# Optimization experiments

Hardware: AMD Instinct MI355X
Metric: run time of the kernel (lower is better)

## Reference

```python
import jax, jax.numpy as jnp
import numpy as np

# H36M 17-joint skeleton: parent-of array
_PARENTS = [-1, 0, 1, 2, 0, 4, 5, 0, 7, 8, 9, 8, 11, 12, 8, 14, 15]

def _make_triplets():
    # (jp, j, jc) for every joint j with a parent jp and child jc
    trips = []
    for jc, j in enumerate(_PARENTS):
        if j <= 0 and j != 0:
            continue
        if j == -1:
            continue
        jp = _PARENTS[j]
        if jp == -1:
            continue
        trips.append((jp, j, jc))
    return trips

TRIPLETS = _make_triplets()  # 12 fixed triplets

B, N, J, C = 16, 243, 17, 512
H, D = 8, C // 8
EPS = 1e-5


def setup_inputs() -> dict:
    key = jax.random.key(0)
    ks = jax.random.split(key, 5)
    s = 1.0 / np.sqrt(C)
    x = jax.random.normal(ks[0], (B, N, J, C), dtype=jnp.float32)
    Wqkv = jax.random.normal(ks[1], (C, 3 * C), dtype=jnp.float32) * s
    bqkv = jax.random.normal(ks[2], (3 * C,), dtype=jnp.float32) * 0.01
    Wproj = jax.random.normal(ks[3], (C, C), dtype=jnp.float32) * s
    bproj = jax.random.normal(ks[4], (C,), dtype=jnp.float32) * 0.01
    return {"x": x, "Wqkv": Wqkv, "bqkv": bqkv, "Wproj": Wproj, "bproj": bproj}


def _hsdm(x, Wqkv, bqkv, Wproj, bproj):
    # x: (B, N, J, C) -> tokens over joints per frame
    xf = x.reshape(B * N, J, C)
    qkv = xf @ Wqkv + bqkv                                   # (BN, J, 3C)
    qkv = qkv.reshape(B * N, J, 3, H, D).transpose(2, 0, 3, 1, 4)  # (3, BN, H, J, D)
    q, k, v = qkv[0], qkv[1], qkv[2]
    scale = 1.0 / jnp.sqrt(jnp.float32(D))
    attn = jax.nn.softmax(jnp.einsum('bhqd,bhkd->bhqk', q, k) * scale, axis=-1)
    # sequential hierarchical adjustment over fixed skeleton triplets
    # (order matters: later triplets read entries written by earlier ones)
    for jp, j, jc in TRIPLETS:
        half = attn[:, :, j, jp] * 0.5
        attn = attn.at[:, :, j, jc].add(half).at[:, :, jc, j].add(half)
    # dropout is identity at inference
    xa = jnp.einsum('bhqk,bhkd->bhqd', attn, v)              # (BN, H, J, D)
    xa = xa.transpose(0, 2, 1, 3).reshape(B * N, J, C)
    xa = xa @ Wproj + bproj
    y = x + xa.reshape(B, N, J, C)
    mu = jnp.mean(y, axis=-1, keepdims=True)
    var = jnp.var(y, axis=-1, keepdims=True)
    return (y - mu) / jnp.sqrt(var + EPS)                     # LN without affine


def reference(x, Wqkv, bqkv, Wproj, bproj):
    return _hsdm(x, Wqkv, bqkv, Wproj, bproj)
```

## Files before the change

kernel.cpp:

```cpp
#include <hip/hip_runtime.h>

typedef unsigned short u16;
typedef unsigned int u32;
typedef short bf16x8 __attribute__((ext_vector_type(8)));
typedef float f32x4 __attribute__((ext_vector_type(4)));
typedef float f32x16 __attribute__((ext_vector_type(16)));

#define M_ROWS   66096
#define M_PAD    66176
#define C_DIM    512
#define NQKV     1536
#define NFRAME   3888


__device__ __forceinline__ u16 f2bf(float f) {
    u32 u = __float_as_uint(f);
    u32 r = (u + 0x7fffu + ((u >> 16) & 1u)) >> 16;
    return (u16)r;
}
__device__ __forceinline__ float bf2f(u16 v) {
    return __uint_as_float(((u32)v) << 16);
}
__device__ __forceinline__ void async16(const void* g, void* l) {
    __builtin_amdgcn_global_load_lds(
        (const __attribute__((address_space(1))) unsigned int*)g,
        (__attribute__((address_space(3))) unsigned int*)l, 16, 0, 0);
}


__global__ __launch_bounds__(256) void cast_x(const float* __restrict__ x, u16* __restrict__ xb) {
    u32 cid = blockIdx.x * 256u + threadIdx.x;
    u32 m  = cid >> 6;
    u32 c0 = (cid & 63u) * 8u;
    if (m >= M_PAD) return;
    u16 v[8];
    if (m < M_ROWS) {
        const float* p = x + (size_t)m * C_DIM + c0;
        float4 f1 = *(const float4*)p;
        float4 f2 = *(const float4*)(p + 4);
        v[0]=f2bf(f1.x); v[1]=f2bf(f1.y); v[2]=f2bf(f1.z); v[3]=f2bf(f1.w);
        v[4]=f2bf(f2.x); v[5]=f2bf(f2.y); v[6]=f2bf(f2.z); v[7]=f2bf(f2.w);
    } else {
        #pragma unroll
        for (int i = 0; i < 8; ++i) v[i] = 0;
    }
    u16* dst = xb + ((size_t)(c0 >> 5) * M_PAD + m) * 32 + (c0 & 31u);
    *(uint4*)dst = *(const uint4*)v;
}


__global__ __launch_bounds__(256) void cast_w(const float* __restrict__ W, u16* __restrict__ out, int N) {
    __shared__ float tile[32 * 65];
    const int n0 = blockIdx.x * 64;
    const int kt = blockIdx.y;
    const int t  = threadIdx.x;
    for (int i = t; i < 2048; i += 256) {
        int k = i >> 6, n = i & 63;
        tile[k * 65 + n] = W[(size_t)(kt * 32 + k) * N + n0 + n];
    }
    __syncthreads();
    {
        int n = t >> 2, kk0 = (t & 3) * 8;
        u16 v[8];
        #pragma unroll
        for (int j = 0; j < 8; ++j) v[j] = f2bf(tile[(kk0 + j) * 65 + n]);
        u16* dst = out + ((size_t)kt * N + n0 + n) * 32 + kk0;
        *(uint4*)dst = *(const uint4*)v;
    }
}


__global__ __launch_bounds__(256) void gemm1(const u16* __restrict__ xb,
                                             const u16* __restrict__ wt,
                                             const float* __restrict__ bqkv,
                                             u16* __restrict__ qkv) {
    __shared__ u16 As[128 * 32];
    __shared__ u16 Bs[128 * 32];
    __shared__ float biasS[128];

    const int n0 = blockIdx.x * 128;
    const int m0 = blockIdx.y * 128;
    const int t  = threadIdx.x;
    const int w  = t >> 6, l = t & 63;
    const int lr = l & 15, lq = l >> 4;
    const int wr = (w >> 1) * 64, wc = (w & 1) * 64;

    if (t < 128) biasS[t] = bqkv[n0 + t];

    f32x4 acc[4][4] = {};

    for (int kt = 0; kt < 16; ++kt) {
        __syncthreads();
        const u16* ga = xb + ((size_t)kt * M_PAD + m0) * 32;
        const u16* gb = wt + ((size_t)kt * NQKV + n0) * 32;
        async16(ga + (size_t)t * 8,         &As[t * 8]);
        async16(ga + (size_t)(t + 256) * 8, &As[(t + 256) * 8]);
        async16(gb + (size_t)t * 8,         &Bs[t * 8]);
        async16(gb + (size_t)(t + 256) * 8, &Bs[(t + 256) * 8]);
        __syncthreads();

        bf16x8 a[4], b[4];
        #pragma unroll
        for (int i = 0; i < 4; ++i) a[i] = *(const bf16x8*)&As[(wr + i * 16 + lr) * 32 + lq * 8];
        #pragma unroll
        for (int i = 0; i < 4; ++i) b[i] = *(const bf16x8*)&Bs[(wc + i * 16 + lr) * 32 + lq * 8];
        #pragma unroll
        for (int i = 0; i < 4; ++i)
            #pragma unroll
            for (int j = 0; j < 4; ++j)
                acc[i][j] = __builtin_amdgcn_mfma_f32_16x16x32_bf16(a[i], b[j], acc[i][j], 0, 0, 0);
    }

    #pragma unroll
    for (int i = 0; i < 4; ++i) {
        #pragma unroll
        for (int j = 0; j < 4; ++j) {
            const int col  = n0 + wc + j * 16 + lr;
            const float bb = biasS[wc + j * 16 + lr];
            #pragma unroll
            for (int r = 0; r < 4; ++r) {
                const int row = m0 + wr + i * 16 + lq * 4 + r;
                if (row < M_ROWS)
                    qkv[(size_t)row * NQKV + col] = f2bf(acc[i][j][r] + bb);
            }
        }
    }
}


__global__ __launch_bounds__(256) void attn_k(const u16* __restrict__ qkv, u16* __restrict__ xa) {
    __shared__ u16 Pb[4][32 * 40];

    const int wv  = threadIdx.x >> 6;
    const int l   = threadIdx.x & 63;
    const int l31 = l & 31;
    const int hi  = l >> 5;

    const int id = blockIdx.x * 4 + wv;
    const int f  = id >> 3;
    const int h  = id & 7;

    const int mrow = (l31 < 17) ? l31 : 0;
    const u16* base = qkv + (size_t)(f * 17) * NQKV;
    const u16* Qp = base + (size_t)mrow * NQKV + h * 64 + 8 * hi;
    const u16* Kp = Qp + 512;

    f32x16 Sacc = {};
    #pragma unroll
    for (int c = 0; c < 4; ++c) {
        bf16x8 aq = *(const bf16x8*)(Qp + 16 * c);
        bf16x8 bk = *(const bf16x8*)(Kp + 16 * c);
        Sacc = __builtin_amdgcn_mfma_f32_32x32x16_bf16(aq, bk, Sacc, 0, 0, 0);
    }

    float p[16];
    #pragma unroll
    for (int r = 0; r < 16; ++r)
        p[r] = (l31 < 17) ? Sacc[r] * 0.125f : -1e30f;

    #pragma unroll
    for (int r = 0; r < 16; ++r) {
        float mx = p[r];
        #pragma unroll
        for (int m = 1; m < 32; m <<= 1) mx = fmaxf(mx, __shfl_xor(mx, m));
        float e = __expf(p[r] - mx);
        float s = e;
        #pragma unroll
        for (int m = 1; m < 32; m <<= 1) s += __shfl_xor(s, m);
        p[r] = e * __builtin_amdgcn_rcpf(s);
    }

    {
        constexpr int TJP[13] = {0,1,0,4,0,7,8,7,8,11,7,8,14};
        constexpr int TJ [13] = {1,2,4,5,7,8,9,8,11,12,8,14,15};
        constexpr int TJC[13] = {2,3,5,6,8,9,10,11,12,13,14,15,16};
        #pragma unroll
        for (int tr = 0; tr < 13; ++tr) {
            const int jp = TJP[tr], j = TJ[tr], jc = TJC[tr];
            const int rj = (j  & 3) | ((j  >> 3) << 2), hj = (j  >> 2) & 1;
            const int rc = (jc & 3) | ((jc >> 3) << 2), hc = (jc >> 2) & 1;
            const float half = 0.5f * __shfl(p[rj], jp + 32 * hj);
            if (l == jc + 32 * hj) p[rj] += half;
            if (l == j  + 32 * hc) p[rc] += half;
        }
    }

    u16* Pw = Pb[wv];
    #pragma unroll
    for (int r = 0; r < 16; ++r) {
        const int row = (r & 3) + 8 * (r >> 2) + 4 * hi;
        Pw[row * 40 + l31] = f2bf(p[r]);
    }
    asm volatile("s_waitcnt lgkmcnt(0)" ::: "memory");

    bf16x8 pa[2];
    #pragma unroll
    for (int c = 0; c < 2; ++c)
        pa[c] = *(const bf16x8*)&Pw[l31 * 40 + 16 * c + 8 * hi];

    const u16* Vbase = base + 1024 + h * 64;
    f32x16 O[2] = {};
    #pragma unroll
    for (int t = 0; t < 2; ++t) {
        #pragma unroll
        for (int c = 0; c < 2; ++c) {
            u16 vv[8];
            #pragma unroll
            for (int j = 0; j < 8; ++j) {
                const int k  = 16 * c + 8 * hi + j;
                const int kr = (k < 17) ? k : 0;
                vv[j] = Vbase[(size_t)kr * NQKV + t * 32 + l31];
            }
            O[t] = __builtin_amdgcn_mfma_f32_32x32x16_bf16(pa[c], *(const bf16x8*)vv, O[t], 0, 0, 0);
        }
    }

    #pragma unroll
    for (int t = 0; t < 2; ++t) {
        const int kt = h * 2 + t;
        #pragma unroll
        for (int r = 0; r < 16; ++r) {
            const int row = (r & 3) + 8 * (r >> 2) + 4 * hi;
            if (row < 17)
                xa[((size_t)kt * M_PAD + (f * 17 + row)) * 32 + l31] = f2bf(O[t][r]);
        }
    }
}


__global__ __launch_bounds__(256) void gemm2_gemm(const u16* __restrict__ xa,
                                                  const u16* __restrict__ wt,
                                                  const float* __restrict__ bproj,
                                                  const float* __restrict__ x,
                                                  float* __restrict__ y) {
    __shared__ u16 As[128 * 32];
    __shared__ u16 Bs[128 * 32];
    __shared__ float biasS[128];

    const int n0 = blockIdx.x * 128;
    const int m0 = blockIdx.y * 128;
    const int t  = threadIdx.x;
    const int w  = t >> 6, l = t & 63;
    const int lr = l & 15, lq = l >> 4;
    const int wr = (w >> 1) * 64, wc = (w & 1) * 64;

    if (t < 128) biasS[t] = bproj[n0 + t];

    f32x4 acc[4][4] = {};

    for (int kt = 0; kt < 16; ++kt) {
        __syncthreads();
        const u16* ga = xa + ((size_t)kt * M_PAD + m0) * 32;
        const u16* gb = wt + ((size_t)kt * C_DIM + n0) * 32;
        async16(ga + (size_t)t * 8,         &As[t * 8]);
        async16(ga + (size_t)(t + 256) * 8, &As[(t + 256) * 8]);
        async16(gb + (size_t)t * 8,         &Bs[t * 8]);
        async16(gb + (size_t)(t + 256) * 8, &Bs[(t + 256) * 8]);
        __syncthreads();

        bf16x8 a[4], b[4];
        #pragma unroll
        for (int i = 0; i < 4; ++i) a[i] = *(const bf16x8*)&As[(wr + i * 16 + lr) * 32 + lq * 8];
        #pragma unroll
        for (int i = 0; i < 4; ++i) b[i] = *(const bf16x8*)&Bs[(wc + i * 16 + lr) * 32 + lq * 8];
        #pragma unroll
        for (int i = 0; i < 4; ++i)
            #pragma unroll
            for (int j = 0; j < 4; ++j)
                acc[i][j] = __builtin_amdgcn_mfma_f32_16x16x32_bf16(a[i], b[j], acc[i][j], 0, 0, 0);
    }

    #pragma unroll
    for (int i = 0; i < 4; ++i) {
        #pragma unroll
        for (int j = 0; j < 4; ++j) {
            const int col  = n0 + wc + j * 16 + lr;
            const float bb = biasS[wc + j * 16 + lr];
            #pragma unroll
            for (int r = 0; r < 4; ++r) {
                const int row = m0 + wr + i * 16 + lq * 4 + r;
                if (row < M_ROWS) {
                    const size_t idx = (size_t)row * C_DIM + col;
                    y[idx] = acc[i][j][r] + bb + x[idx];
                }
            }
        }
    }
}


__global__ __launch_bounds__(256) void ln_k(const float* __restrict__ y, float* __restrict__ out) {
    const int row = blockIdx.x * 4 + (threadIdx.x >> 6);
    const int l   = threadIdx.x & 63;
    const float* p = y + (size_t)row * C_DIM + l * 8;
    float4 a = *(const float4*)p;
    float4 b = *(const float4*)(p + 4);
    float s  = a.x + a.y + a.z + a.w + b.x + b.y + b.z + b.w;
    float sq = a.x*a.x + a.y*a.y + a.z*a.z + a.w*a.w
             + b.x*b.x + b.y*b.y + b.z*b.z + b.w*b.w;
    #pragma unroll
    for (int m = 1; m < 64; m <<= 1) {
        s  += __shfl_xor(s, m);
        sq += __shfl_xor(sq, m);
    }
    const float mean = s * (1.f / 512.f);
    const float var  = sq * (1.f / 512.f) - mean * mean;
    const float rstd = rsqrtf(var + 1e-5f);
    float* q = out + (size_t)row * C_DIM + l * 8;
    float4 o1, o2;
    o1.x = (a.x - mean) * rstd; o1.y = (a.y - mean) * rstd;
    o1.z = (a.z - mean) * rstd; o1.w = (a.w - mean) * rstd;
    o2.x = (b.x - mean) * rstd; o2.y = (b.y - mean) * rstd;
    o2.z = (b.z - mean) * rstd; o2.w = (b.w - mean) * rstd;
    *(float4*)q = o1;
    *(float4*)(q + 4) = o2;
}


extern "C" void kernel_launch(void* const* d_in, const int* in_sizes, int n_in,
                              void* d_out, int out_size, void* d_ws, size_t ws_size,
                              hipStream_t stream) {
    const float* x     = (const float*)d_in[0];
    const float* Wqkv  = (const float*)d_in[1];
    const float* bqkv  = (const float*)d_in[2];
    const float* Wproj = (const float*)d_in[3];
    const float* bproj = (const float*)d_in[4];
    float* out = (float*)d_out;

    u16* xb  = (u16*)d_ws;
    u16* wqt = xb  + (size_t)M_PAD * C_DIM;
    u16* wpt = wqt + (size_t)NQKV * C_DIM;
    u16* qkv = wpt + (size_t)C_DIM * C_DIM;
    u16* xa  = qkv + (size_t)M_PAD * NQKV;
    float* y = (float*)qkv;

    cast_x<<<(M_PAD * 64) / 256, 256, 0, stream>>>(x, xb);
    cast_w<<<dim3(NQKV / 64, 16), 256, 0, stream>>>(Wqkv, wqt, NQKV);
    cast_w<<<dim3(C_DIM / 64, 16), 256, 0, stream>>>(Wproj, wpt, C_DIM);
    gemm1<<<dim3(NQKV / 128, M_PAD / 128), 256, 0, stream>>>(xb, wqt, bqkv, qkv);
    attn_k<<<(NFRAME * 8) / 4, 256, 0, stream>>>(qkv, xa);
    gemm2_gemm<<<dim3(C_DIM / 128, M_PAD / 128), 256, 0, stream>>>(xa, wpt, bproj, x, y);
    ln_k<<<M_ROWS / 4, 256, 0, stream>>>(y, out);
}
```

Measured before the change: 650.2 us.

## Fuse projection GEMM with LayerNorm and double-buffer QKV GEMM loads

The output-projection GEMM now computes full 512-wide rows per block, with 32 rows per block and each of 4 waves owning 128 columns. It loads operands directly from global memory into registers and applies bias, residual and LayerNorm in the epilogue using shuffle and shared-memory reductions. This removes the separate fp32 y round trip and the LN kernel launch. The QKV GEMM gets double-buffered LDS staging so the next K tile is prefetched while MFMAs run on the current one. The risks are gemm2 losing LDS reuse (the weight tile is re-read from global or L2 by every block) and a single barrier per iteration in the pipelined loop.

```diff
diff --git a/kernel.cpp b/kernel.cpp
--- a/kernel.cpp
+++ b/kernel.cpp
@@ -74,8 +74,8 @@
                                              const u16* __restrict__ wt,
                                              const float* __restrict__ bqkv,
                                              u16* __restrict__ qkv) {
-    __shared__ u16 As[128 * 32];
-    __shared__ u16 Bs[128 * 32];
+    __shared__ u16 As[2][128 * 32];
+    __shared__ u16 Bs[2][128 * 32];
     __shared__ float biasS[128];
 
     const int n0 = blockIdx.x * 128;
@@ -89,26 +89,34 @@
 
     f32x4 acc[4][4] = {};
 
-    for (int kt = 0; kt < 16; ++kt) {
-        __syncthreads();
+    auto stage = [&](int kt, int bi) {
         const u16* ga = xb + ((size_t)kt * M_PAD + m0) * 32;
         const u16* gb = wt + ((size_t)kt * NQKV + n0) * 32;
-        async16(ga + (size_t)t * 8,         &As[t * 8]);
-        async16(ga + (size_t)(t + 256) * 8, &As[(t + 256) * 8]);
-        async16(gb + (size_t)t * 8,         &Bs[t * 8]);
-        async16(gb + (size_t)(t + 256) * 8, &Bs[(t + 256) * 8]);
-        __syncthreads();
+        async16(ga + (size_t)t * 8,         &As[bi][t * 8]);
+        async16(ga + (size_t)(t + 256) * 8, &As[bi][(t + 256) * 8]);
+        async16(gb + (size_t)t * 8,         &Bs[bi][t * 8]);
+        async16(gb + (size_t)(t + 256) * 8, &Bs[bi][(t + 256) * 8]);
+    };
+
+    stage(0, 0);
+    __syncthreads();
+
+    for (int kt = 0; kt < 16; ++kt) {
+        const int cur = kt & 1;
+        if (kt < 15) stage(kt + 1, cur ^ 1);
 
         bf16x8 a[4], b[4];
         #pragma unroll
-        for (int i = 0; i < 4; ++i) a[i] = *(const bf16x8*)&As[(wr + i * 16 + lr) * 32 + lq * 8];
-        #pragma unroll
-        for (int i = 0; i < 4; ++i) b[i] = *(const bf16x8*)&Bs[(wc + i * 16 + lr) * 32 + lq * 8];
+        for (int i = 0; i < 4; ++i) a[i] = *(const bf16x8*)&As[cur][(wr + i * 16 + lr) * 32 + lq * 8];
+        #pragma unroll
+        for (int i = 0; i < 4; ++i) b[i] = *(const bf16x8*)&Bs[cur][(wc + i * 16 + lr) * 32 + lq * 8];
         #pragma unroll
         for (int i = 0; i < 4; ++i)
             #pragma unroll
             for (int j = 0; j < 4; ++j)
                 acc[i][j] = __builtin_amdgcn_mfma_f32_16x16x32_bf16(a[i], b[j], acc[i][j], 0, 0, 0);
+
+        __syncthreads();
     }
 
     #pragma unroll
@@ -228,92 +236,105 @@
 }
 
 
-__global__ __launch_bounds__(256) void gemm2_gemm(const u16* __restrict__ xa,
-                                                  const u16* __restrict__ wt,
-                                                  const float* __restrict__ bproj,
-                                                  const float* __restrict__ x,
-                                                  float* __restrict__ y) {
-    __shared__ u16 As[128 * 32];
-    __shared__ u16 Bs[128 * 32];
-    __shared__ float biasS[128];
-
-    const int n0 = blockIdx.x * 128;
-    const int m0 = blockIdx.y * 128;
+__global__ __launch_bounds__(256) void gemm2_ln(const u16* __restrict__ xa,
+                                                const u16* __restrict__ wt,
+                                                const float* __restrict__ bproj,
+                                                const float* __restrict__ x,
+                                                float* __restrict__ out) {
+    __shared__ float part[32][4][2];
+
+    const int m0 = blockIdx.x * 32;
     const int t  = threadIdx.x;
-    const int w  = t >> 6, l = t & 63;
+    const int wn = t >> 6, l = t & 63;
     const int lr = l & 15, lq = l >> 4;
-    const int wr = (w >> 1) * 64, wc = (w & 1) * 64;
-
-    if (t < 128) biasS[t] = bproj[n0 + t];
-
-    f32x4 acc[4][4] = {};
-
+
+    f32x4 acc[2][8] = {};
+
+    #pragma unroll 2
     for (int kt = 0; kt < 16; ++kt) {
-        __syncthreads();
-        const u16* ga = xa + ((size_t)kt * M_PAD + m0) * 32;
-        const u16* gb = wt + ((size_t)kt * C_DIM + n0) * 32;
-        async16(ga + (size_t)t * 8,         &As[t * 8]);
-        async16(ga + (size_t)(t + 256) * 8, &As[(t + 256) * 8]);
-        async16(gb + (size_t)t * 8,         &Bs[t * 8]);
-        async16(gb + (size_t)(t + 256) * 8, &Bs[(t + 256) * 8]);
-        __syncthreads();
-
-        bf16x8 a[4], b[4];
-        #pragma unroll
-        for (int i = 0; i < 4; ++i) a[i] = *(const bf16x8*)&As[(wr + i * 16 + lr) * 32 + lq * 8];
-        #pragma unroll
-        for (int i = 0; i < 4; ++i) b[i] = *(const bf16x8*)&Bs[(wc + i * 16 + lr) * 32 + lq * 8];
-        #pragma unroll
-        for (int i = 0; i < 4; ++i)
-            #pragma unroll
-            for (int j = 0; j < 4; ++j)
+        const u16* ga = xa + ((size_t)kt * M_PAD + m0 + lr) * 32 + lq * 8;
+        const u16* gb = wt + ((size_t)kt * C_DIM + wn * 128 + lr) * 32 + lq * 8;
+        bf16x8 a[2], b[8];
+        #pragma unroll
+        for (int i = 0; i < 2; ++i) a[i] = *(const bf16x8*)(ga + (size_t)i * 16 * 32);
+        #pragma unroll
+        for (int j = 0; j < 8; ++j) b[j] = *(const bf16x8*)(gb + (size_t)j * 16 * 32);
+        #pragma unroll
+        for (int i = 0; i < 2; ++i)
+            #pragma unroll
+            for (int j = 0; j < 8; ++j)
                 acc[i][j] = __builtin_amdgcn_mfma_f32_16x16x32_bf16(a[i], b[j], acc[i][j], 0, 0, 0);
     }
 
-    #pragma unroll
-    for (int i = 0; i < 4; ++i) {
-        #pragma unroll
-        for (int j = 0; j < 4; ++j) {
-            const int col  = n0 + wc + j * 16 + lr;
-            const float bb = biasS[wc + j * 16 + lr];
+    float bias[8];
+    #pragma unroll
+    for (int j = 0; j < 8; ++j) bias[j] = bproj[wn * 128 + j * 16 + lr];
+
+    float s[2][4], sq[2][4];
+    #pragma unroll
+    for (int i = 0; i < 2; ++i)
+        #pragma unroll
+        for (int r = 0; r < 4; ++r) { s[i][r] = 0.f; sq[i][r] = 0.f; }
+
+    #pragma unroll
+    for (int i = 0; i < 2; ++i) {
+        #pragma unroll
+        for (int r = 0; r < 4; ++r) {
+            const int rowg = m0 + i * 16 + lq * 4 + r;
+            const bool valid = rowg < M_ROWS;
+            const float* xr = x + (size_t)rowg * C_DIM + wn * 128 + lr;
+            #pragma unroll
+            for (int j = 0; j < 8; ++j) {
+                float v = acc[i][j][r] + bias[j];
+                if (valid) v += xr[j * 16];
+                acc[i][j][r] = v;
+                s[i][r]  += v;
+                sq[i][r] += v * v;
+            }
+        }
+    }
+
+    #pragma unroll
+    for (int i = 0; i < 2; ++i)
+        #pragma unroll
+        for (int r = 0; r < 4; ++r)
+            #pragma unroll
+            for (int m = 1; m < 16; m <<= 1) {
+                s[i][r]  += __shfl_xor(s[i][r],  m);
+                sq[i][r] += __shfl_xor(sq[i][r], m);
+            }
+
+    if (lr == 0) {
+        #pragma unroll
+        for (int i = 0; i < 2; ++i)
             #pragma unroll
             for (int r = 0; r < 4; ++r) {
-                const int row = m0 + wr + i * 16 + lq * 4 + r;
-                if (row < M_ROWS) {
-                    const size_t idx = (size_t)row * C_DIM + col;
-                    y[idx] = acc[i][j][r] + bb + x[idx];
-                }
-            }
-        }
-    }
-}
-
-
-__global__ __launch_bounds__(256) void ln_k(const float* __restrict__ y, float* __restrict__ out) {
-    const int row = blockIdx.x * 4 + (threadIdx.x >> 6);
-    const int l   = threadIdx.x & 63;
-    const float* p = y + (size_t)row * C_DIM + l * 8;
-    float4 a = *(const float4*)p;
-    float4 b = *(const float4*)(p + 4);
-    float s  = a.x + a.y + a.z + a.w + b.x + b.y + b.z + b.w;
-    float sq = a.x*a.x + a.y*a.y + a.z*a.z + a.w*a.w
-             + b.x*b.x + b.y*b.y + b.z*b.z + b.w*b.w;
-    #pragma unroll
-    for (int m = 1; m < 64; m <<= 1) {
-        s  += __shfl_xor(s, m);
-        sq += __shfl_xor(sq, m);
-    }
-    const float mean = s * (1.f / 512.f);
-    const float var  = sq * (1.f / 512.f) - mean * mean;
-    const float rstd = rsqrtf(var + 1e-5f);
-    float* q = out + (size_t)row * C_DIM + l * 8;
-    float4 o1, o2;
-    o1.x = (a.x - mean) * rstd; o1.y = (a.y - mean) * rstd;
-    o1.z = (a.z - mean) * rstd; o1.w = (a.w - mean) * rstd;
-    o2.x = (b.x - mean) * rstd; o2.y = (b.y - mean) * rstd;
-    o2.z = (b.z - mean) * rstd; o2.w = (b.w - mean) * rstd;
-    *(float4*)q = o1;
-    *(float4*)(q + 4) = o2;
+                const int rl = i * 16 + lq * 4 + r;
+                part[rl][wn][0] = s[i][r];
+                part[rl][wn][1] = sq[i][r];
+            }
+    }
+    __syncthreads();
+
+    #pragma unroll
+    for (int i = 0; i < 2; ++i) {
+        #pragma unroll
+        for (int r = 0; r < 4; ++r) {
+            const int rl   = i * 16 + lq * 4 + r;
+            const int rowg = m0 + rl;
+            const float ss = part[rl][0][0] + part[rl][1][0] + part[rl][2][0] + part[rl][3][0];
+            const float qq = part[rl][0][1] + part[rl][1][1] + part[rl][2][1] + part[rl][3][1];
+            const float mean = ss * (1.f / 512.f);
+            const float var  = qq * (1.f / 512.f) - mean * mean;
+            const float rstd = rsqrtf(var + 1e-5f);
+            if (rowg < M_ROWS) {
+                float* orow = out + (size_t)rowg * C_DIM + wn * 128 + lr;
+                #pragma unroll
+                for (int j = 0; j < 8; ++j)
+                    orow[j * 16] = (acc[i][j][r] - mean) * rstd;
+            }
+        }
+    }
 }
 
 
@@ -332,13 +353,11 @@
     u16* wpt = wqt + (size_t)NQKV * C_DIM;
     u16* qkv = wpt + (size_t)C_DIM * C_DIM;
     u16* xa  = qkv + (size_t)M_PAD * NQKV;
-    float* y = (float*)qkv;
 
     cast_x<<<(M_PAD * 64) / 256, 256, 0, stream>>>(x, xb);
     cast_w<<<dim3(NQKV / 64, 16), 256, 0, stream>>>(Wqkv, wqt, NQKV);
     cast_w<<<dim3(C_DIM / 64, 16), 256, 0, stream>>>(Wproj, wpt, C_DIM);
     gemm1<<<dim3(NQKV / 128, M_PAD / 128), 256, 0, stream>>>(xb, wqt, bqkv, qkv);
     attn_k<<<(NFRAME * 8) / 4, 256, 0, stream>>>(qkv, xa);
-    gemm2_gemm<<<dim3(C_DIM / 128, M_PAD / 128), 256, 0, stream>>>(xa, wpt, bproj, x, y);
-    ln_k<<<M_ROWS / 4, 256, 0, stream>>>(y, out);
-}
+    gemm2_ln<<<(M_ROWS + 31) / 32, 256, 0, stream>>>(xa, wpt, bproj, x, out);
+}
```

After: 680.4 us. 4.6% more time.
